# Kernel optimization log

Hardware: AMD Instinct MI355X
Metric: run time of the kernel (lower is better)

The kernel has to match this reference:

```python
import jax, jax.numpy as jnp
import numpy as np

B, T, I = 256, 1024, 64
P, E, NOUT = 256, 128, 64
K = 2
TEMP = 8.0
LN_EPS = 1e-5


def setup_inputs() -> dict:
    key = jax.random.key(0)
    ks = jax.random.split(key, 10)
    lim_in = 1.0 / np.sqrt(I)
    lim_e = 1.0 / np.sqrt(E)
    return {
        "x": jax.random.normal(ks[0], (B, T, I), dtype=jnp.float32),
        "pointer_init": jax.random.uniform(ks[1], (B,), dtype=jnp.float32) * P,
        "W_in": jax.random.uniform(ks[2], (E, I), minval=-lim_in, maxval=lim_in),
        "b_in": jax.random.uniform(ks[3], (E,), minval=-lim_in, maxval=lim_in),
        "ln_w": jnp.ones((E,), jnp.float32),
        "ln_b": jnp.zeros((E,), jnp.float32),
        "jump_dest": jax.random.uniform(ks[4], (P,), dtype=jnp.float32) * P,
        "Wg": jax.random.uniform(ks[5], (1, E), minval=-lim_e, maxval=lim_e),
        "bg": jax.random.uniform(ks[6], (1,), minval=-lim_e, maxval=lim_e),
        "context_strength": jnp.float32(0.2),
        "Wo": jax.random.uniform(ks[7], (NOUT, E), minval=-lim_e, maxval=lim_e),
        "bo": jax.random.uniform(ks[8], (NOUT,), minval=-lim_e, maxval=lim_e),
    }


def _layer_norm(h, w, b):
    mu = jnp.mean(h, axis=-1, keepdims=True)
    var = jnp.mean((h - mu) ** 2, axis=-1, keepdims=True)
    return (h - mu) * jax.lax.rsqrt(var + LN_EPS) * w + b


def reference(x, pointer_init, W_in, b_in, ln_w, ln_b, jump_dest, Wg, bg, context_strength, Wo, bo):
    Bsz = x.shape[0]
    nP = jump_dest.shape[0]
    offsets = jnp.arange(-K, K + 1, dtype=jnp.int32)  # [5]
    batch_idx = jnp.arange(Bsz)[:, None]               # [B,1]
    ctx_scale = jax.nn.sigmoid(context_strength)
    half = nP / 2.0

    def step(carry, x_t):
        mem, hid, ptr = carry                          # [B,P,E], [B,E], [B]
        emb = jnp.tanh(x_t @ W_in.T + b_in)            # [B,E]
        base = jnp.clip(jnp.floor(ptr).astype(jnp.int32), 0, nP - 1)
        idx = jnp.mod(base[:, None] + offsets[None, :], nP)  # [B,5]
        delta = jnp.mod(idx.astype(x_t.dtype) - ptr[:, None] + half, nP) - half
        w = jax.nn.softmax(-(delta ** 2) / TEMP, axis=1)     # [B,5]
        nbh = jnp.take_along_axis(mem, idx[:, :, None], axis=1)  # [B,5,E]
        ctx = jnp.sum(w[:, :, None] * nbh, axis=1)               # [B,E]
        su = jnp.tanh(emb + ctx_scale * ctx + hid)               # [B,E]
        hid_new = _layer_norm(su, ln_w, ln_b)
        mem_new = mem.at[batch_idx, idx].add(w[:, :, None] * su[:, None, :])
        cur = jnp.clip(ptr.astype(jnp.int32), 0, nP - 1)
        jt = jump_dest[cur]                                      # [B]
        jl = (su @ Wg.T + bg)[:, 0]                              # [B]
        probs = jax.nn.sigmoid(jl)
        sj = (probs > 0.5).astype(x_t.dtype) - jax.lax.stop_gradient(probs) + probs
        walk = jnp.mod(ptr + 1.0, nP)
        ptr_new = jnp.where(sj > 0.5, jt, walk)
        return (mem_new, hid_new, ptr_new), None

    mem0 = jnp.zeros((Bsz, nP, W_in.shape[0]), x.dtype)
    hid0 = jnp.zeros((Bsz, W_in.shape[0]), x.dtype)
    (mem, hid, ptr), _ = jax.lax.scan(step, (mem0, hid0, pointer_init), jnp.swapaxes(x, 0, 1))
    logits = hid @ Wo.T + bo
    return logits
```

## Files before the change

kernel.cpp:

```cpp
#include <hip/hip_runtime.h>
#include <math.h>

#define Bn    256
#define Tn    1024
#define In    64
#define Pn    256
#define En    128
#define NOUTn 64
#define LN_EPS 1e-5f

#define C1f 0.3606737602222409f
#define K1f 0.8824969025845955f
#define K2f 0.6065306597126334f

typedef float f32x2 __attribute__((ext_vector_type(2)));

__device__ __forceinline__ float tanh_fast(float x) {
    float e = __builtin_amdgcn_exp2f(x * 2.88539008177793f);
    return 1.0f - 2.0f * __builtin_amdgcn_rcpf(e + 1.0f);
}
__device__ __forceinline__ f32x2 tanh2(f32x2 x) {
    f32x2 e;
    e[0] = __builtin_amdgcn_exp2f(x[0] * 2.88539008177793f);
    e[1] = __builtin_amdgcn_exp2f(x[1] * 2.88539008177793f);
    f32x2 r;
    r[0] = __builtin_amdgcn_rcpf(e[0] + 1.0f);
    r[1] = __builtin_amdgcn_rcpf(e[1] + 1.0f);
    return 1.0f - 2.0f * r;
}

template<int CTRL, int RMASK>
__device__ __forceinline__ float dpp_add(float x) {
    return x + __int_as_float(__builtin_amdgcn_update_dpp(
        0, __float_as_int(x), CTRL, RMASK, 0xF, false));
}
__device__ __forceinline__ void wave_sum64_x3(float& x, float& y, float& z) {
#define LVL(C, R) x = dpp_add<C, R>(x); y = dpp_add<C, R>(y); z = dpp_add<C, R>(z);
    LVL(0x111, 0xF)
    LVL(0x112, 0xF)
    LVL(0x114, 0xF)
    LVL(0x118, 0xF)
    LVL(0x142, 0xA)
    LVL(0x143, 0xC)
#undef LVL
    x = __int_as_float(__builtin_amdgcn_readlane(__float_as_int(x), 63));
    y = __int_as_float(__builtin_amdgcn_readlane(__float_as_int(y), 63));
    z = __int_as_float(__builtin_amdgcn_readlane(__float_as_int(z), 63));
}

__global__ __launch_bounds__(256)
void embgemm_kernel(const float* __restrict__ x, const float* __restrict__ W_in,
                    const float* __restrict__ b_in, float* __restrict__ emb4) {
    __shared__ float wlds[128 * 68];
    const int tid = threadIdx.x;
    for (int i = tid; i < 128 * 64; i += 256)
        wlds[(i >> 6) * 68 + (i & 63)] = W_in[i];
    __syncthreads();

    const int b    = blockIdx.x >> 3;
    const int tseg = blockIdx.x & 7;
    const int w    = tid >> 6;
    const int l    = tid & 63;
    const int t0   = tseg * 128 + (w >> 1) * 64 + (l >> 3) * 8;
    const int e0   = (w & 1) * 64 + (l & 7);

    float acc[8][8];
    #pragma unroll
    for (int i = 0; i < 8; ++i)
        #pragma unroll
        for (int j = 0; j < 8; ++j) acc[i][j] = 0.f;

    const float4* xrow = (const float4*)(x + ((size_t)b * Tn + t0) * In);

    for (int i4 = 0; i4 < 16; ++i4) {
        float4 xv[8];
        #pragma unroll
        for (int tt = 0; tt < 8; ++tt) xv[tt] = xrow[tt * 16 + i4];
        float4 wf[8];
        #pragma unroll
        for (int j = 0; j < 8; ++j)
            wf[j] = *(const float4*)&wlds[(e0 + 8 * j) * 68 + i4 * 4];
        #pragma unroll
        for (int tt = 0; tt < 8; ++tt)
            #pragma unroll
            for (int j = 0; j < 8; ++j) {
                acc[tt][j] += xv[tt].x * wf[j].x;
                acc[tt][j] += xv[tt].y * wf[j].y;
                acc[tt][j] += xv[tt].z * wf[j].z;
                acc[tt][j] += xv[tt].w * wf[j].w;
            }
    }

    const int tb0 = t0 >> 2;
    #pragma unroll
    for (int j = 0; j < 8; ++j) {
        const int e = e0 + 8 * j;
        const float be = b_in[e];
        #pragma unroll
        for (int tb = 0; tb < 2; ++tb) {
            float4 o;
            o.x = tanh_fast(acc[tb * 4 + 0][j] + be);
            o.y = tanh_fast(acc[tb * 4 + 1][j] + be);
            o.z = tanh_fast(acc[tb * 4 + 2][j] + be);
            o.w = tanh_fast(acc[tb * 4 + 3][j] + be);
            *(float4*)&emb4[(((size_t)b * 256 + tb0 + tb) * 128 + e) * 4] = o;
        }
    }
}

#define LDSG_FLOATS (Pn * En + Pn)
#define LDSG_BYTES  (LDSG_FLOATS * 4)

__global__ __launch_bounds__(64, 1)
void scan4_kernel(const float* __restrict__ emb4,
                  const float* __restrict__ pointer_init,
                  const float* __restrict__ ln_w, const float* __restrict__ ln_b,
                  const float* __restrict__ jump_dest,
                  const float* __restrict__ Wg,  const float* __restrict__ bg,
                  const float* __restrict__ cs_ptr,
                  const float* __restrict__ Wo,  const float* __restrict__ bo,
                  float* __restrict__ out) {
    extern __shared__ float lds[];
    float* mem = lds;
    float* jd  = lds + Pn * En;

    const int b = blockIdx.x;
    const int l = threadIdx.x;

    float4* m4 = (float4*)mem;
    for (int i = l; i < Pn * En / 4; i += 64) m4[i] = make_float4(0.f, 0.f, 0.f, 0.f);
    for (int i = l; i < Pn; i += 64) jd[i] = jump_dest[i];

    const f32x2 lnw = {ln_w[l], ln_w[l + 64]};
    const f32x2 lnb = {ln_b[l], ln_b[l + 64]};
    const f32x2 wg  = {Wg[l],   Wg[l + 64]};
    const float bgs = bg[0];
    const float cs  = 1.0f / (1.0f + expf(-cs_ptr[0]));
    f32x2 hid = {0.f, 0.f};

    float* myb = mem + 2 * l;

    const float4* e40 = (const float4*)(emb4 + ((size_t)b << 17)) + l;
    const float4* e41 = e40 + 64;
    float4 A0 = e40[0],   A1 = e41[0];
    float4 B0 = e40[128], B1 = e41[128];

    float jl     = 1.0f;
    float jt_cur = pointer_init[b];
    float ptrW   = 0.f;
    int   baseW  = 0;
    float jtW_pre = 0.f;
    float z0 = 0.f, z1 = 0.f, z2 = 1.f, z3 = 0.f, z4 = 0.f, inv = 1.f;
    f32x2 wnb0 = {0,0}, wnb1 = {0,0}, wnb2 = {0,0}, wnb3 = {0,0}, wnb4 = {0,0};
    float *wp0 = myb, *wp1 = myb, *wp2 = myb, *wp3 = myb, *wp4 = myb;

#define SSTEP(EC0, EC1) {                                                      \
    float ptr; int base;                                                       \
    f32x2 nb0, nb1, nb2, nb3, nb4;                                             \
    float *p0, *p1, *p2, *p3, *p4;                                             \
    float jt_nxt;                                                              \
    if (__builtin_amdgcn_readfirstlane(__float_as_int(jl)) > 0) {              \
                                     \
        ptr  = jt_cur;                                                         \
        base = (int)ptr; base = base > 255 ? 255 : base;                       \
        p0 = mem + (((base + 254) & 255) << 7) + 2 * l;                        \
        p1 = mem + (((base + 255) & 255) << 7) + 2 * l;                        \
        p2 = mem + (base << 7) + 2 * l;                                        \
        p3 = mem + (((base + 1) & 255) << 7) + 2 * l;                          \
        p4 = mem + (((base + 2) & 255) << 7) + 2 * l;                          \
        nb0 = *(f32x2*)p0; nb1 = *(f32x2*)p1; nb2 = *(f32x2*)p2;               \
        nb3 = *(f32x2*)p3; nb4 = *(f32x2*)p4;                                  \
        jt_nxt = jd[base];                                                     \
        const float frac = ptr - (float)base;                                  \
        const float r  = __builtin_amdgcn_exp2f(frac * C1f);                   \
        const float ri = __builtin_amdgcn_exp2f(-frac * C1f);                  \
        z0 = K2f * ri * ri; z1 = K1f * ri; z2 = 1.0f;                          \
        z3 = K1f * r;       z4 = K2f * r * r;                                  \
        inv = __builtin_amdgcn_rcpf(((z0 + z1) + (z2 + z3)) + z4);             \
    } else {                                                                   \
          \
        ptr = ptrW; base = baseW;                                              \
        nb0 = wnb0; nb1 = wnb1; nb2 = wnb2; nb3 = wnb3; nb4 = wnb4;            \
        p0 = wp0; p1 = wp1; p2 = wp2; p3 = wp3; p4 = wp4;                      \
        jt_nxt = jtW_pre;                                                      \
    }                                                                          \
    const f32x2 ctx = inv * (((nb0 * z0 + nb1 * z1) + (nb2 * z2 + nb3 * z3))   \
                             + nb4 * z4);                                      \
    f32x2 em; em[0] = (EC0); em[1] = (EC1);                                    \
    const f32x2 su = tanh2(em + cs * ctx + hid);                               \
    const f32x2 g  = su * inv;                                                 \
    const f32x2 m0v = nb0 + z0 * g, m1v = nb1 + z1 * g, m2v = nb2 + z2 * g,    \
                m3v = nb3 + z3 * g, m4v = nb4 + z4 * g;                        \
    *(f32x2*)p0 = m0v; *(f32x2*)p1 = m1v; *(f32x2*)p2 = m2v;                   \
    *(f32x2*)p3 = m3v; *(f32x2*)p4 = m4v;                                      \
     \
    baseW = (base + 1) & 255;                                                  \
    ptrW  = ptr + 1.0f; if (ptrW >= 256.0f) ptrW -= 256.0f;                    \
    wnb0 = m1v; wnb1 = m2v; wnb2 = m3v; wnb3 = m4v;                            \
    wp0 = p1; wp1 = p2; wp2 = p3; wp3 = p4;                                    \
    wp4 = mem + (((base + 3) & 255) << 7) + 2 * l;                             \
    wnb4 = *(f32x2*)wp4;                                                       \
    jtW_pre = jd[baseW];                                                       \
    jt_cur  = jt_nxt;                                                          \
                                                   \
    float s1 = su[0] + su[1];                                                  \
    const f32x2 sq = su * su;  float s2 = sq[0] + sq[1];                       \
    const f32x2 sg = su * wg;  float s3 = sg[0] + sg[1];                       \
    wave_sum64_x3(s1, s2, s3);                                                 \
    const float mu   = s1 * (1.0f / En);                                       \
    const float var  = s2 * (1.0f / En) - mu * mu;                             \
    const float rstd = __builtin_amdgcn_rsqf(var + LN_EPS);                    \
    hid = (su - mu) * rstd * lnw + lnb;                                        \
    jl  = s3 + bgs;                                                            \
}

    for (int tb = 0; tb < 256; ++tb) {
        const int tp = tb + 2 > 255 ? 255 : tb + 2;
        float4 C0 = e40[tp << 7];
        float4 C1 = e41[tp << 7];
        SSTEP(A0.x, A1.x)
        SSTEP(A0.y, A1.y)
        SSTEP(A0.z, A1.z)
        SSTEP(A0.w, A1.w)
        A0 = B0; A1 = B1; B0 = C0; B1 = C1;
    }
#undef SSTEP

    mem[l] = hid[0]; mem[64 + l] = hid[1];
    __syncthreads();
    const float4* w4 = (const float4*)(Wo + l * En);
    const float4* h4 = (const float4*)mem;
    float a0 = 0.f, a1 = 0.f, a2 = 0.f, a3 = 0.f;
    #pragma unroll
    for (int i = 0; i < En / 4; ++i) {
        float4 wv = w4[i]; float4 hv = h4[i];
        a0 += wv.x * hv.x; a1 += wv.y * hv.y; a2 += wv.z * hv.z; a3 += wv.w * hv.w;
    }
    out[b * NOUTn + l] = (a0 + a1) + (a2 + a3) + bo[l];
}

#define LDS_FLOATS (Pn*En + 2*En + 2*In + Pn)
#define LDS_BYTES  (LDS_FLOATS * 4)

__global__ __launch_bounds__(192, 1)
void ring_kernel(const float* __restrict__ x,
                 const float* __restrict__ pointer_init,
                 const float* __restrict__ W_in,
                 const float* __restrict__ b_in,
                 const float* __restrict__ ln_w,
                 const float* __restrict__ ln_b,
                 const float* __restrict__ jump_dest,
                 const float* __restrict__ Wg,
                 const float* __restrict__ bg,
                 const float* __restrict__ cs_ptr,
                 const float* __restrict__ Wo,
                 const float* __restrict__ bo,
                 float* __restrict__ out)
{
    extern __shared__ float lds[];
    float* mem  = lds;
    float* embb = mem + Pn * En;
    float* xb   = embb + 2 * En;
    float* jd   = xb + 2 * In;

    const int b   = blockIdx.x;
    const int tid = threadIdx.x;

    for (int i = tid; i < Pn * En; i += 192) mem[i] = 0.0f;
    for (int i = tid; i < Pn;      i += 192) jd[i]  = jump_dest[i];

    const float* xrow = x + (size_t)b * Tn * In;
    if (tid < 64) {
        xb[tid]      = xrow[tid];
        xb[In + tid] = xrow[In + tid];
    }
    __syncthreads();

    if (tid >= 64) {
        const int p = tid - 64;
        float wr[In];
        {
            const float4* w4 = (const float4*)(W_in + p * In);
            #pragma unroll
            for (int i = 0; i < In / 4; ++i) {
                float4 v = w4[i];
                wr[4*i+0] = v.x; wr[4*i+1] = v.y; wr[4*i+2] = v.z; wr[4*i+3] = v.w;
            }
        }
        const float bi = b_in[p];
        {
            float acc = bi;
            #pragma unroll
            for (int i = 0; i < In; ++i) acc += wr[i] * xb[i];
            embb[p] = tanhf(acc);
        }
        __syncthreads();
        for (int t = 0; t < Tn; ++t) {
            if (t + 1 < Tn) {
                const float* xc = xb + ((t + 1) & 1) * In;
                float acc = bi;
                #pragma unroll
                for (int i = 0; i < In; ++i) acc += wr[i] * xc[i];
                embb[((t + 1) & 1) * En + p] = tanhf(acc);
            }
            __syncthreads();
        }
    } else {
        const int l = tid;
        const float lnw0 = ln_w[l],      lnw1 = ln_w[l + 64];
        const float lnb0 = ln_b[l],      lnb1 = ln_b[l + 64];
        const float wg0  = Wg[l],        wg1  = Wg[l + 64];
        const float bgs  = bg[0];
        const float cs   = 1.0f / (1.0f + expf(-cs_ptr[0]));
        float hid0 = 0.0f, hid1 = 0.0f;
        float ptr  = pointer_init[b];
        __syncthreads();

        for (int t = 0; t < Tn; ++t) {
            const bool do_stage = (t + 2 < Tn);
            float xs = 0.0f;
            if (do_stage) xs = xrow[(t + 2) * In + l];

            const float* embc = embb + (t & 1) * En;

            int base = (int)floorf(ptr);
            base = base < 0 ? 0 : (base > Pn - 1 ? Pn - 1 : base);
            int cur = (int)ptr;
            cur = cur < 0 ? 0 : (cur > Pn - 1 ? Pn - 1 : cur);
            const float jt = jd[cur];

            const float frac = ptr - (float)base;
            int   idx[5];
            float wgt[5];
            float mx = -3.4e38f;
            #pragma unroll
            for (int j = 0; j < 5; ++j) {
                idx[j] = (base + j - 2 + Pn) & (Pn - 1);
                float d = (float)(j - 2) - frac;
                float s = -(d * d) * 0.125f;
                wgt[j] = s;
                mx = fmaxf(mx, s);
            }
            float se = 0.0f;
            #pragma unroll
            for (int j = 0; j < 5; ++j) { float ez = expf(wgt[j] - mx); wgt[j] = ez; se += ez; }
            const float inv = 1.0f / se;

            float nb0[5], nb1[5];
            #pragma unroll
            for (int j = 0; j < 5; ++j) {
                nb0[j] = mem[idx[j] * En + l];
                nb1[j] = mem[idx[j] * En + 64 + l];
            }
            float ctx0 = 0.0f, ctx1 = 0.0f;
            #pragma unroll
            for (int j = 0; j < 5; ++j) {
                const float w = wgt[j] * inv; wgt[j] = w;
                ctx0 += w * nb0[j];
                ctx1 += w * nb1[j];
            }

            const float su0 = tanhf(embc[l]      + cs * ctx0 + hid0);
            const float su1 = tanhf(embc[l + 64] + cs * ctx1 + hid1);

            #pragma unroll
            for (int j = 0; j < 5; ++j) {
                mem[idx[j] * En + l]      = nb0[j] + wgt[j] * su0;
                mem[idx[j] * En + 64 + l] = nb1[j] + wgt[j] * su1;
            }

            float s1 = su0 + su1;
            float s2 = su0 * su0 + su1 * su1;
            float s3 = su0 * wg0 + su1 * wg1;
            #pragma unroll
            for (int off = 32; off > 0; off >>= 1) {
                s1 += __shfl_xor(s1, off, 64);
                s2 += __shfl_xor(s2, off, 64);
                s3 += __shfl_xor(s3, off, 64);
            }

            const float mu   = s1 * (1.0f / En);
            const float var  = s2 * (1.0f / En) - mu * mu;
            const float rstd = rsqrtf(var + LN_EPS);
            hid0 = (su0 - mu) * rstd * lnw0 + lnb0;
            hid1 = (su1 - mu) * rstd * lnw1 + lnb1;

            const float jl = s3 + bgs;
            float walk = ptr + 1.0f;
            if (walk >= 256.0f) walk -= 256.0f;
            ptr = (jl > 0.0f) ? jt : walk;

            if (do_stage) xb[(t & 1) * In + l] = xs;
            __syncthreads();
        }
        embb[l]      = hid0;
        embb[l + 64] = hid1;
    }
    __syncthreads();

    if (tid < NOUTn) {
        const float* wrow = Wo + tid * En;
        float acc = bo[tid];
        #pragma unroll 4
        for (int e = 0; e < En; ++e) acc += embb[e] * wrow[e];
        out[b * NOUTn + tid] = acc;
    }
}

extern "C" void kernel_launch(void* const* d_in, const int* in_sizes, int n_in,
                              void* d_out, int out_size, void* d_ws, size_t ws_size,
                              hipStream_t stream) {
    const float* x            = (const float*)d_in[0];
    const float* pointer_init = (const float*)d_in[1];
    const float* W_in         = (const float*)d_in[2];
    const float* b_in         = (const float*)d_in[3];
    const float* ln_w         = (const float*)d_in[4];
    const float* ln_b         = (const float*)d_in[5];
    const float* jump_dest    = (const float*)d_in[6];
    const float* Wg           = (const float*)d_in[7];
    const float* bg           = (const float*)d_in[8];
    const float* cs           = (const float*)d_in[9];
    const float* Wo           = (const float*)d_in[10];
    const float* bo           = (const float*)d_in[11];
    float* out = (float*)d_out;

    const size_t emb_bytes = (size_t)Bn * Tn * En * sizeof(float);

    if (ws_size >= emb_bytes) {
        float* emb4 = (float*)d_ws;
        embgemm_kernel<<<Bn * 8, 256, 0, stream>>>(x, W_in, b_in, emb4);
        (void)hipFuncSetAttribute((const void*)scan4_kernel,
                                  hipFuncAttributeMaxDynamicSharedMemorySize, LDSG_BYTES);
        scan4_kernel<<<Bn, 64, LDSG_BYTES, stream>>>(
            emb4, pointer_init, ln_w, ln_b, jump_dest, Wg, bg, cs, Wo, bo, out);
    } else {
        (void)hipFuncSetAttribute((const void*)ring_kernel,
                                  hipFuncAttributeMaxDynamicSharedMemorySize, LDS_BYTES);
        ring_kernel<<<Bn, 192, LDS_BYTES, stream>>>(
            x, pointer_init, W_in, b_in, ln_w, ln_b, jump_dest, Wg, bg, cs, Wo, bo, out);
    }
}
```

Measured before the change: 519.6 us.

## Speculatively precompute jump-target neighbourhood and weights off the critical path

Each step now loads the 5-row neighbourhood and computes the softmax weights for the jump destination of the current position, before the gate decision is known. At the next step it just selects between the walk state and this precomputed jump state. The intent is to take the dependent LDS loads and exp work after a jump off the serial per-step chain, so the gate decision only picks registers. In exchange every step does 5 extra LDS reads and 2 extra exp2 even when no jump happens, and the branch becomes a select on a per-lane float instead of a readfirstlane.

```diff
diff --git a/kernel.cpp b/kernel.cpp
--- a/kernel.cpp
+++ b/kernel.cpp
@@ -112,7 +112,7 @@
 #define LDSG_BYTES  (LDSG_FLOATS * 4)
 
 __global__ __launch_bounds__(64, 1)
-void scan4_kernel(const float* __restrict__ emb4,
+void scan5_kernel(const float* __restrict__ emb4,
                   const float* __restrict__ pointer_init,
                   const float* __restrict__ ln_w, const float* __restrict__ ln_b,
                   const float* __restrict__ jump_dest,
@@ -138,70 +138,70 @@
     const float cs  = 1.0f / (1.0f + expf(-cs_ptr[0]));
     f32x2 hid = {0.f, 0.f};
 
-    float* myb = mem + 2 * l;
-
     const float4* e40 = (const float4*)(emb4 + ((size_t)b << 17)) + l;
     const float4* e41 = e40 + 64;
     float4 A0 = e40[0],   A1 = e41[0];
     float4 B0 = e40[128], B1 = e41[128];
 
-    float jl     = 1.0f;
-    float jt_cur = pointer_init[b];
-    float ptrW   = 0.f;
-    int   baseW  = 0;
-    float jtW_pre = 0.f;
-    float z0 = 0.f, z1 = 0.f, z2 = 1.f, z3 = 0.f, z4 = 0.f, inv = 1.f;
-    f32x2 wnb0 = {0,0}, wnb1 = {0,0}, wnb2 = {0,0}, wnb3 = {0,0}, wnb4 = {0,0};
-    float *wp0 = myb, *wp1 = myb, *wp2 = myb, *wp3 = myb, *wp4 = myb;
+    float ptr = 0.f; int base = 0;
+    float z0 = 0.f, z1 = 0.f, z3 = 0.f, z4 = 0.f, inv = 1.f;
+    f32x2 nb0 = {0,0}, nb1 = {0,0}, nb2 = {0,0}, nb3 = {0,0}, nb4 = {0,0};
+
+    float jl      = 1.0f;
+    float jmp_ptr = pointer_init[b];
+    int   jmp_base = (int)jmp_ptr; jmp_base = jmp_base > 255 ? 255 : jmp_base;
+    float zJ0, zJ1, zJ3, zJ4, invJ;
+    {
+        const float fj = jmp_ptr - (float)jmp_base;
+        const float rj  = __builtin_amdgcn_exp2f(fj * C1f);
+        const float rji = __builtin_amdgcn_exp2f(-fj * C1f);
+        zJ0 = K2f * rji * rji; zJ1 = K1f * rji;
+        zJ3 = K1f * rj;        zJ4 = K2f * rj * rj;
+        invJ = __builtin_amdgcn_rcpf(((zJ0 + zJ1) + (1.0f + zJ3)) + zJ4);
+    }
+    f32x2 nbJ0 = {0,0}, nbJ1 = {0,0}, nbJ2 = {0,0}, nbJ3 = {0,0}, nbJ4 = {0,0};
 
 #define SSTEP(EC0, EC1) {                                                      \
-    float ptr; int base;                                                       \
-    f32x2 nb0, nb1, nb2, nb3, nb4;                                             \
-    float *p0, *p1, *p2, *p3, *p4;                                             \
-    float jt_nxt;                                                              \
-    if (__builtin_amdgcn_readfirstlane(__float_as_int(jl)) > 0) {              \
-                                     \
-        ptr  = jt_cur;                                                         \
-        base = (int)ptr; base = base > 255 ? 255 : base;                       \
-        p0 = mem + (((base + 254) & 255) << 7) + 2 * l;                        \
-        p1 = mem + (((base + 255) & 255) << 7) + 2 * l;                        \
-        p2 = mem + (base << 7) + 2 * l;                                        \
-        p3 = mem + (((base + 1) & 255) << 7) + 2 * l;                          \
-        p4 = mem + (((base + 2) & 255) << 7) + 2 * l;                          \
-        nb0 = *(f32x2*)p0; nb1 = *(f32x2*)p1; nb2 = *(f32x2*)p2;               \
-        nb3 = *(f32x2*)p3; nb4 = *(f32x2*)p4;                                  \
-        jt_nxt = jd[base];                                                     \
-        const float frac = ptr - (float)base;                                  \
-        const float r  = __builtin_amdgcn_exp2f(frac * C1f);                   \
-        const float ri = __builtin_amdgcn_exp2f(-frac * C1f);                  \
-        z0 = K2f * ri * ri; z1 = K1f * ri; z2 = 1.0f;                          \
-        z3 = K1f * r;       z4 = K2f * r * r;                                  \
-        inv = __builtin_amdgcn_rcpf(((z0 + z1) + (z2 + z3)) + z4);             \
-    } else {                                                                   \
-          \
-        ptr = ptrW; base = baseW;                                              \
-        nb0 = wnb0; nb1 = wnb1; nb2 = wnb2; nb3 = wnb3; nb4 = wnb4;            \
-        p0 = wp0; p1 = wp1; p2 = wp2; p3 = wp3; p4 = wp4;                      \
-        jt_nxt = jtW_pre;                                                      \
+    if (jl > 0.0f) {    \
+        ptr = jmp_ptr; base = jmp_base;                                        \
+        z0 = zJ0; z1 = zJ1; z3 = zJ3; z4 = zJ4; inv = invJ;                    \
+        nb0 = nbJ0; nb1 = nbJ1; nb2 = nbJ2; nb3 = nbJ3; nb4 = nbJ4;            \
     }                                                                          \
-    const f32x2 ctx = inv * (((nb0 * z0 + nb1 * z1) + (nb2 * z2 + nb3 * z3))   \
+    const float jtN = jd[base];                   \
+    float* r0 = mem + (((base + 254) & 255) << 7) + 2 * l;                     \
+    float* r1 = mem + (((base + 255) & 255) << 7) + 2 * l;                     \
+    float* r2 = mem + ((base) << 7) + 2 * l;                                   \
+    float* r3 = mem + (((base + 1) & 255) << 7) + 2 * l;                       \
+    float* r4 = mem + (((base + 2) & 255) << 7) + 2 * l;                       \
+    const f32x2 ctx = inv * (((nb0 * z0 + nb1 * z1) + (nb2 + nb3 * z3))        \
                              + nb4 * z4);                                      \
     f32x2 em; em[0] = (EC0); em[1] = (EC1);                                    \
     const f32x2 su = tanh2(em + cs * ctx + hid);                               \
     const f32x2 g  = su * inv;                                                 \
-    const f32x2 m0v = nb0 + z0 * g, m1v = nb1 + z1 * g, m2v = nb2 + z2 * g,    \
+    const f32x2 m0v = nb0 + z0 * g, m1v = nb1 + z1 * g, m2v = nb2 + g,         \
                 m3v = nb3 + z3 * g, m4v = nb4 + z4 * g;                        \
-    *(f32x2*)p0 = m0v; *(f32x2*)p1 = m1v; *(f32x2*)p2 = m2v;                   \
-    *(f32x2*)p3 = m3v; *(f32x2*)p4 = m4v;                                      \
-     \
-    baseW = (base + 1) & 255;                                                  \
-    ptrW  = ptr + 1.0f; if (ptrW >= 256.0f) ptrW -= 256.0f;                    \
-    wnb0 = m1v; wnb1 = m2v; wnb2 = m3v; wnb3 = m4v;                            \
-    wp0 = p1; wp1 = p2; wp2 = p3; wp3 = p4;                                    \
-    wp4 = mem + (((base + 3) & 255) << 7) + 2 * l;                             \
-    wnb4 = *(f32x2*)wp4;                                                       \
-    jtW_pre = jd[baseW];                                                       \
-    jt_cur  = jt_nxt;                                                          \
+    *(f32x2*)r0 = m0v; *(f32x2*)r1 = m1v; *(f32x2*)r2 = m2v;                   \
+    *(f32x2*)r3 = m3v; *(f32x2*)r4 = m4v;                                      \
+          \
+    nb0 = m1v; nb1 = m2v; nb2 = m3v; nb3 = m4v;                                \
+    nb4 = *(f32x2*)(mem + (((base + 3) & 255) << 7) + 2 * l);                  \
+    ptr = ptr + 1.0f; if (ptr >= 256.0f) ptr -= 256.0f;                        \
+    base = (base + 1) & 255;                                                   \
+    \
+    jmp_ptr = jtN;                                                             \
+    int bj = (int)jtN; bj = bj > 255 ? 255 : bj;                               \
+    jmp_base = bj;                                                             \
+    nbJ0 = *(f32x2*)(mem + (((bj + 254) & 255) << 7) + 2 * l);                 \
+    nbJ1 = *(f32x2*)(mem + (((bj + 255) & 255) << 7) + 2 * l);                 \
+    nbJ2 = *(f32x2*)(mem + ((bj) << 7) + 2 * l);                               \
+    nbJ3 = *(f32x2*)(mem + (((bj + 1) & 255) << 7) + 2 * l);                   \
+    nbJ4 = *(f32x2*)(mem + (((bj + 2) & 255) << 7) + 2 * l);                   \
+    const float fj = jtN - (float)bj;                                          \
+    const float rj  = __builtin_amdgcn_exp2f(fj * C1f);                        \
+    const float rji = __builtin_amdgcn_exp2f(-fj * C1f);                       \
+    zJ0 = K2f * rji * rji; zJ1 = K1f * rji;                                    \
+    zJ3 = K1f * rj;        zJ4 = K2f * rj * rj;                                \
+    invJ = __builtin_amdgcn_rcpf(((zJ0 + zJ1) + (1.0f + zJ3)) + zJ4);          \
                                                    \
     float s1 = su[0] + su[1];                                                  \
     const f32x2 sq = su * su;  float s2 = sq[0] + sq[1];                       \
@@ -429,9 +429,9 @@
     if (ws_size >= emb_bytes) {
         float* emb4 = (float*)d_ws;
         embgemm_kernel<<<Bn * 8, 256, 0, stream>>>(x, W_in, b_in, emb4);
-        (void)hipFuncSetAttribute((const void*)scan4_kernel,
+        (void)hipFuncSetAttribute((const void*)scan5_kernel,
                                   hipFuncAttributeMaxDynamicSharedMemorySize, LDSG_BYTES);
-        scan4_kernel<<<Bn, 64, LDSG_BYTES, stream>>>(
+        scan5_kernel<<<Bn, 64, LDSG_BYTES, stream>>>(
             emb4, pointer_init, ln_w, ln_b, jump_dest, Wg, bg, cs, Wo, bo, out);
     } else {
         (void)hipFuncSetAttribute((const void*)ring_kernel,
```

Result: slower. 533.7 us (+2.7%).

## Fuse embedding GEMM into scan kernel with producer waves overlapping the recurrence

Applied to the files above, without the earlier changes.

Replaces the separate embedding GEMM kernel with two extra producer waves inside the scan kernel's workgroup. Each producer thread computes one embedding channel for chunks of 64 timesteps, two chunks ahead, into the global workspace. Per-chunk __syncthreads hand the data to the single scan wave. This hides the GEMM behind the serial recurrence and removes a kernel launch. In exchange the GEMM now runs on only 128 threads per batch row without LDS tiling, and the scan wave pays a barrier every 64 steps.

```diff
diff --git a/kernel.cpp b/kernel.cpp
--- a/kernel.cpp
+++ b/kernel.cpp
@@ -48,84 +48,69 @@
     z = __int_as_float(__builtin_amdgcn_readlane(__float_as_int(z), 63));
 }
 
-__global__ __launch_bounds__(256)
-void embgemm_kernel(const float* __restrict__ x, const float* __restrict__ W_in,
-                    const float* __restrict__ b_in, float* __restrict__ emb4) {
-    __shared__ float wlds[128 * 68];
-    const int tid = threadIdx.x;
-    for (int i = tid; i < 128 * 64; i += 256)
-        wlds[(i >> 6) * 68 + (i & 63)] = W_in[i];
-    __syncthreads();
-
-    const int b    = blockIdx.x >> 3;
-    const int tseg = blockIdx.x & 7;
-    const int w    = tid >> 6;
-    const int l    = tid & 63;
-    const int t0   = tseg * 128 + (w >> 1) * 64 + (l >> 3) * 8;
-    const int e0   = (w & 1) * 64 + (l & 7);
-
-    float acc[8][8];
-    #pragma unroll
-    for (int i = 0; i < 8; ++i)
-        #pragma unroll
-        for (int j = 0; j < 8; ++j) acc[i][j] = 0.f;
-
-    const float4* xrow = (const float4*)(x + ((size_t)b * Tn + t0) * In);
-
-    for (int i4 = 0; i4 < 16; ++i4) {
-        float4 xv[8];
-        #pragma unroll
-        for (int tt = 0; tt < 8; ++tt) xv[tt] = xrow[tt * 16 + i4];
-        float4 wf[8];
-        #pragma unroll
-        for (int j = 0; j < 8; ++j)
-            wf[j] = *(const float4*)&wlds[(e0 + 8 * j) * 68 + i4 * 4];
-        #pragma unroll
-        for (int tt = 0; tt < 8; ++tt)
-            #pragma unroll
-            for (int j = 0; j < 8; ++j) {
-                acc[tt][j] += xv[tt].x * wf[j].x;
-                acc[tt][j] += xv[tt].y * wf[j].y;
-                acc[tt][j] += xv[tt].z * wf[j].z;
-                acc[tt][j] += xv[tt].w * wf[j].w;
-            }
-    }
-
-    const int tb0 = t0 >> 2;
-    #pragma unroll
-    for (int j = 0; j < 8; ++j) {
-        const int e = e0 + 8 * j;
-        const float be = b_in[e];
-        #pragma unroll
-        for (int tb = 0; tb < 2; ++tb) {
-            float4 o;
-            o.x = tanh_fast(acc[tb * 4 + 0][j] + be);
-            o.y = tanh_fast(acc[tb * 4 + 1][j] + be);
-            o.z = tanh_fast(acc[tb * 4 + 2][j] + be);
-            o.w = tanh_fast(acc[tb * 4 + 3][j] + be);
-            *(float4*)&emb4[(((size_t)b * 256 + tb0 + tb) * 128 + e) * 4] = o;
-        }
-    }
-}
-
-#define LDSG_FLOATS (Pn * En + Pn)
-#define LDSG_BYTES  (LDSG_FLOATS * 4)
-
-__global__ __launch_bounds__(64, 1)
-void scan4_kernel(const float* __restrict__ emb4,
+#define LDSF_FLOATS (Pn * En + Pn)
+#define LDSF_BYTES  (LDSF_FLOATS * 4)
+
+__global__ __launch_bounds__(192, 1)
+void fused_kernel(const float* __restrict__ x,
                   const float* __restrict__ pointer_init,
+                  const float* __restrict__ W_in, const float* __restrict__ b_in,
                   const float* __restrict__ ln_w, const float* __restrict__ ln_b,
                   const float* __restrict__ jump_dest,
                   const float* __restrict__ Wg,  const float* __restrict__ bg,
                   const float* __restrict__ cs_ptr,
                   const float* __restrict__ Wo,  const float* __restrict__ bo,
-                  float* __restrict__ out) {
+                  float* __restrict__ emb4, float* __restrict__ out) {
     extern __shared__ float lds[];
     float* mem = lds;
     float* jd  = lds + Pn * En;
 
-    const int b = blockIdx.x;
-    const int l = threadIdx.x;
+    const int b   = blockIdx.x;
+    const int tid = threadIdx.x;
+
+    if (tid >= 64) {
+        const int e = tid - 64;
+        float w[In];
+        {
+            const float4* w4 = (const float4*)(W_in + e * In);
+            #pragma unroll
+            for (int i = 0; i < 16; ++i) {
+                float4 v = w4[i];
+                w[4*i] = v.x; w[4*i+1] = v.y; w[4*i+2] = v.z; w[4*i+3] = v.w;
+            }
+        }
+        const float be = b_in[e];
+        const float* xb  = x + (size_t)b * Tn * In;
+        float*       dst = emb4 + ((size_t)b << 17);
+
+#define PRODUCE(K) {                                                     \
+    for (int tt = 0; tt < 64; ++tt) {                                    \
+        const int t = (K) * 64 + tt;                                     \
+        const float4* xr = (const float4*)(xb + t * In);                 \
+        float a0 = 0.f, a1 = 0.f, a2 = 0.f, a3 = 0.f;                    \
+        _Pragma("unroll")                                                \
+        for (int i = 0; i < 16; ++i) {                                   \
+            float4 xv = xr[i];                                           \
+            a0 += xv.x * w[4*i];   a1 += xv.y * w[4*i+1];                \
+            a2 += xv.z * w[4*i+2]; a3 += xv.w * w[4*i+3];                \
+        }                                                                \
+        dst[((t >> 2) * 128 + e) * 4 + (t & 3)] =                        \
+            tanh_fast((a0 + a1) + (a2 + a3) + be);                       \
+    }                                                                    \
+}
+        PRODUCE(0)
+        PRODUCE(1)
+        __syncthreads();
+        for (int k = 0; k < 16; ++k) {
+            if (k + 2 < 16) PRODUCE(k + 2)
+            __syncthreads();
+        }
+#undef PRODUCE
+        __syncthreads();
+        return;
+    }
+
+    const int l = tid;
 
     float4* m4 = (float4*)mem;
     for (int i = l; i < Pn * En / 4; i += 64) m4[i] = make_float4(0.f, 0.f, 0.f, 0.f);
@@ -140,19 +125,21 @@
 
     float* myb = mem + 2 * l;
 
+    float jl      = 1.0f;
+    float jt_cur  = pointer_init[b];
+    float ptrW    = 0.f;
+    int   baseW   = 0;
+    float jtW_pre = 0.f;
+    float z0 = 0.f, z1 = 0.f, z2 = 1.f, z3 = 0.f, z4 = 0.f, inv = 1.f;
+    f32x2 wnb0 = {0,0}, wnb1 = {0,0}, wnb2 = {0,0}, wnb3 = {0,0}, wnb4 = {0,0};
+    float *wp0 = myb, *wp1 = myb, *wp2 = myb, *wp3 = myb, *wp4 = myb;
+
+    __syncthreads();
+
     const float4* e40 = (const float4*)(emb4 + ((size_t)b << 17)) + l;
     const float4* e41 = e40 + 64;
     float4 A0 = e40[0],   A1 = e41[0];
     float4 B0 = e40[128], B1 = e41[128];
-
-    float jl     = 1.0f;
-    float jt_cur = pointer_init[b];
-    float ptrW   = 0.f;
-    int   baseW  = 0;
-    float jtW_pre = 0.f;
-    float z0 = 0.f, z1 = 0.f, z2 = 1.f, z3 = 0.f, z4 = 0.f, inv = 1.f;
-    f32x2 wnb0 = {0,0}, wnb1 = {0,0}, wnb2 = {0,0}, wnb3 = {0,0}, wnb4 = {0,0};
-    float *wp0 = myb, *wp1 = myb, *wp2 = myb, *wp3 = myb, *wp4 = myb;
 
 #define SSTEP(EC0, EC1) {                                                      \
     float ptr; int base;                                                       \
@@ -214,15 +201,19 @@
     jl  = s3 + bgs;                                                            \
 }
 
-    for (int tb = 0; tb < 256; ++tb) {
-        const int tp = tb + 2 > 255 ? 255 : tb + 2;
-        float4 C0 = e40[tp << 7];
-        float4 C1 = e41[tp << 7];
-        SSTEP(A0.x, A1.x)
-        SSTEP(A0.y, A1.y)
-        SSTEP(A0.z, A1.z)
-        SSTEP(A0.w, A1.w)
-        A0 = B0; A1 = B1; B0 = C0; B1 = C1;
+    for (int k = 0; k < 16; ++k) {
+        for (int tbi = 0; tbi < 16; ++tbi) {
+            const int tb = k * 16 + tbi;
+            const int tp = tb + 2 > 255 ? 255 : tb + 2;
+            float4 C0 = e40[tp << 7];
+            float4 C1 = e41[tp << 7];
+            SSTEP(A0.x, A1.x)
+            SSTEP(A0.y, A1.y)
+            SSTEP(A0.z, A1.z)
+            SSTEP(A0.w, A1.w)
+            A0 = B0; A1 = B1; B0 = C0; B1 = C1;
+        }
+        __syncthreads();
     }
 #undef SSTEP
 
@@ -428,11 +419,11 @@
 
     if (ws_size >= emb_bytes) {
         float* emb4 = (float*)d_ws;
-        embgemm_kernel<<<Bn * 8, 256, 0, stream>>>(x, W_in, b_in, emb4);
-        (void)hipFuncSetAttribute((const void*)scan4_kernel,
-                                  hipFuncAttributeMaxDynamicSharedMemorySize, LDSG_BYTES);
-        scan4_kernel<<<Bn, 64, LDSG_BYTES, stream>>>(
-            emb4, pointer_init, ln_w, ln_b, jump_dest, Wg, bg, cs, Wo, bo, out);
+        (void)hipFuncSetAttribute((const void*)fused_kernel,
+                                  hipFuncAttributeMaxDynamicSharedMemorySize, LDSF_BYTES);
+        fused_kernel<<<Bn, 192, LDSF_BYTES, stream>>>(
+            x, pointer_init, W_in, b_in, ln_w, ln_b, jump_dest, Wg, bg, cs,
+            Wo, bo, emb4, out);
     } else {
         (void)hipFuncSetAttribute((const void*)ring_kernel,
                                   hipFuncAttributeMaxDynamicSharedMemorySize, LDS_BYTES);
```

After: 746.2 us. +43.6%, slower.
